# Kernel tuning notes

Measured on AMD Instinct MI355X. Metric: run time of the kernel, lower is better.

## Reference

```python
import jax, jax.numpy as jnp
import numpy as np

EMBED = 768; HEADS = 12; DH = 64; DEPTH = 6; MLP = 3072
PATCH = (4, 16, 16)
N_PATCH = 2048          # (32/4)*(256/16)*(256/16)
N_REAL = N_PATCH + 1    # + cls token
S_PAD = 4096            # padded to multiple of max segment length
SEGS = [128, 256, 512, 1024, 2048]
RATIOS = [1, 2, 4, 8, 16]
NEG = -1e9


def _ln(x, w, b, eps=1e-5):
    m = jnp.mean(x, -1, keepdims=True)
    v = jnp.mean((x - m) ** 2, -1, keepdims=True)
    return (x - m) / jnp.sqrt(v + eps) * w + b


def dilated_attn(x, wq, bq, wk, bk, wv, bv, wo, bo):
    """LongNet dilated attention: per (segment w, ratio r) branch, split the
    sequence into segments of length w, keep every r-th token with a per-head
    offset (h % r), run dense attention inside the sparse segment, then combine
    branches per position/head with softmax-denominator (lse) weights."""
    B, S, E = x.shape
    q = (x @ wq + bq).reshape(B, S, HEADS, DH)
    k = (x @ wk + bk).reshape(B, S, HEADS, DH)
    v = (x @ wv + bv).reshape(B, S, HEADS, DH)
    scale = 1.0 / np.sqrt(DH).astype(np.float32)
    harr = jnp.arange(HEADS)[:, None]
    outs, lses = [], []
    for w, r in zip(SEGS, RATIOS):
        ns, m = S // w, w // r
        idx = (jnp.arange(HEADS)[:, None] % r) + r * jnp.arange(m)[None, :]  # [H, m]

        def seg(t):
            t = t.reshape(B, ns, w, HEADS, DH).transpose(0, 1, 3, 2, 4)  # B,ns,H,w,D
            return jnp.take_along_axis(t, idx[None, None, :, :, None], axis=3)

        qs, ks, vs = seg(q), seg(k), seg(v)  # [B, ns, H, m, D]
        pos = (jnp.arange(ns) * w)[:, None, None] + idx[None]  # [ns, H, m]
        kmask = jnp.where(pos < N_REAL, 0.0, NEG)  # mask padded keys
        sc = jnp.einsum('bnhqd,bnhkd->bnhqk', qs, ks) * scale + kmask[None, :, :, None, :]
        lse = jax.nn.logsumexp(sc, axis=-1)  # [B, ns, H, m]
        o = jnp.einsum('bnhqk,bnhkd->bnhqd', jax.nn.softmax(sc, axis=-1), vs)
        of = jnp.zeros((B, ns, HEADS, w, DH), x.dtype).at[:, :, harr, idx, :].set(o)
        lf = jnp.full((B, ns, HEADS, w), NEG, x.dtype).at[:, :, harr, idx].set(lse)
        outs.append(of.transpose(0, 1, 3, 2, 4).reshape(B, S, HEADS, DH))
        lses.append(lf.transpose(0, 1, 3, 2).reshape(B, S, HEADS))
    O = jnp.stack(outs)   # [Br, B, S, H, D]
    L = jnp.stack(lses)   # [Br, B, S, H]
    wts = jnp.exp(L - jnp.max(L, 0))
    wts = wts / jnp.sum(wts, 0)
    out = jnp.sum(O * wts[..., None], 0).reshape(B, S, E)
    return out @ wo + bo


def setup_inputs() -> dict:
    key = jax.random.key(0)
    ks = jax.random.split(key, 16)
    f = lambda k, shape: (0.02 * jax.random.normal(k, shape)).astype(jnp.float32)
    z = lambda *s: jnp.zeros(s, jnp.float32)
    o = lambda *s: jnp.ones(s, jnp.float32)
    return {
        'x': jax.random.normal(ks[0], (1, 1, 32, 256, 256), dtype=jnp.float32),
        'conv_w': f(ks[1], (EMBED, 1) + PATCH),
        'conv_b': z(EMBED),
        'cls_token': f(ks[2], (1, 1, EMBED)),
        'pos_embed': f(ks[3], (1, N_REAL, EMBED)),
        'ln1_w': o(DEPTH, EMBED), 'ln1_b': z(DEPTH, EMBED),
        'wq': f(ks[4], (DEPTH, EMBED, EMBED)), 'bq': z(DEPTH, EMBED),
        'wk': f(ks[5], (DEPTH, EMBED, EMBED)), 'bk': z(DEPTH, EMBED),
        'wv': f(ks[6], (DEPTH, EMBED, EMBED)), 'bv': z(DEPTH, EMBED),
        'wo': f(ks[7], (DEPTH, EMBED, EMBED)), 'bo': z(DEPTH, EMBED),
        'ln2_w': o(DEPTH, EMBED), 'ln2_b': z(DEPTH, EMBED),
        'w1': f(ks[8], (DEPTH, EMBED, MLP)), 'b1': z(DEPTH, MLP),
        'w2': f(ks[9], (DEPTH, MLP, EMBED)), 'b2': z(DEPTH, EMBED),
        'lnf_w': o(EMBED), 'lnf_b': z(EMBED),
    }


def reference(x, conv_w, conv_b, cls_token, pos_embed, ln1_w, ln1_b,
              wq, bq, wk, bk, wv, bv, wo, bo, ln2_w, ln2_b,
              w1, b1, w2, b2, lnf_w, lnf_b):
    # 3D patch embed: Conv3d stride=kernel=patch, then flatten spatial -> tokens
    p = jax.lax.conv_general_dilated(
        x, conv_w, window_strides=PATCH, padding='VALID',
        dimension_numbers=('NCDHW', 'OIDHW', 'NCDHW'))
    p = p + conv_b[None, :, None, None, None]
    B = p.shape[0]
    tok = p.reshape(B, EMBED, -1).transpose(0, 2, 1)  # [B, N_PATCH, E]
    tok = tok + pos_embed[:, 1:, :]
    cls = cls_token + pos_embed[:, :1, :]
    h = jnp.concatenate([jnp.broadcast_to(cls, (B, 1, EMBED)), tok], axis=1)
    h = jnp.pad(h, ((0, 0), (0, S_PAD - N_REAL), (0, 0)))  # pad to segment multiple

    params = {'ln1_w': ln1_w, 'ln1_b': ln1_b, 'wq': wq, 'bq': bq, 'wk': wk,
              'bk': bk, 'wv': wv, 'bv': bv, 'wo': wo, 'bo': bo,
              'ln2_w': ln2_w, 'ln2_b': ln2_b, 'w1': w1, 'b1': b1,
              'w2': w2, 'b2': b2}

    def layer(h, pr):
        a = dilated_attn(_ln(h, pr['ln1_w'], pr['ln1_b']),
                         pr['wq'], pr['bq'], pr['wk'], pr['bk'],
                         pr['wv'], pr['bv'], pr['wo'], pr['bo'])
        h = h + a
        f = _ln(h, pr['ln2_w'], pr['ln2_b'])
        f = jax.nn.gelu(f @ pr['w1'] + pr['b1'], approximate=False) @ pr['w2'] + pr['b2']
        return h + f, None

    h, _ = jax.lax.scan(layer, h, params)
    return _ln(h[:, 0], lnf_w, lnf_b)  # [B, EMBED]
```

## Files before the change

### kernel.cpp

```cpp
#include <hip/hip_runtime.h>
#include <math.h>

#define EMBED 768
#define HEADS 12
#define DH 64
#define DEPTH 6
#define MLP_DIM 3072
#define N_REAL 2049
#define SP 2112
#define SPAD 2176
#define NEGV (-1e9f)

typedef __attribute__((ext_vector_type(8))) short short8;
typedef __attribute__((ext_vector_type(4))) float f32x4;

__device__ __forceinline__ unsigned short f2bf(float f) {
    union { float f; unsigned u; } x; x.f = f;
    unsigned r = x.u + 0x7FFF + ((x.u >> 16) & 1);
    return (unsigned short)(r >> 16);
}
__device__ __forceinline__ float bf2f(unsigned short s) {
    union { unsigned u; float f; } x; x.u = (unsigned)s << 16;
    return x.f;
}

__device__ __forceinline__ size_t pidx(int mj, int k, int nkt) {
    return (((size_t)(mj >> 4) * nkt + (k >> 5)) << 9) + (size_t)((((k >> 3) & 3) * 16 + (mj & 15)) * 8 + (k & 7));
}

__global__ void im2col_kernel(const float* __restrict__ x, unsigned short* __restrict__ p) {
    const int pi = blockIdx.x;
    const int d = pi >> 8, rr = (pi >> 4) & 15, cc = pi & 15;
    const int t = threadIdx.x;
    #pragma unroll
    for (int u = 0; u < 4; ++u) {
        int i = u * 256 + t;
        int kd = i >> 8, kr = (i >> 4) & 15, kc = i & 15;
        float v = x[(size_t)(d * 4 + kd) * 65536 + (rr * 16 + kr) * 256 + (cc * 16 + kc)];
        p[pidx(pi, i, 32)] = f2bf(v);
    }
}

__device__ __forceinline__ void pack_KN_body(const float* __restrict__ src,
                                             unsigned short* __restrict__ dst,
                                             int N, int K, int bn, int bk) {
    __shared__ float lf[128][33];
    const int t = threadIdx.x;
    {
        const int kk = t >> 3, ch = t & 7;
        const float4* s = (const float4*)(src + (size_t)(bk * 32 + kk) * N + bn * 128 + ch * 16);
        float4 v0 = s[0], v1 = s[1], v2 = s[2], v3 = s[3];
        float tmp[16];
        ((float4*)tmp)[0] = v0; ((float4*)tmp)[1] = v1; ((float4*)tmp)[2] = v2; ((float4*)tmp)[3] = v3;
        #pragma unroll
        for (int u = 0; u < 16; ++u) lf[ch * 16 + u][kk] = tmp[u];
    }
    __syncthreads();
    const int nkt = K >> 5;
    const int cg = t >> 5;
    const int l0 = (t & 31) * 2;
    unsigned short* o = dst + (((size_t)(bn * 8 + cg) * nkt + bk) << 9);
    #pragma unroll
    for (int q = 0; q < 2; ++q) {
        const int l = l0 + q;
        const int col = cg * 16 + (l & 15), kb = (l >> 4) * 8;
        unsigned short ov[8];
        #pragma unroll
        for (int e = 0; e < 8; ++e) ov[e] = f2bf(lf[col][kb + e]);
        *(short8*)(o + l * 8) = *(short8*)ov;
    }
}

__device__ __forceinline__ void pack_piece(int r,
                                           const float* wq, const float* wk,
                                           const float* wv, const float* wo,
                                           const float* w1s, const float* w2s,
                                           unsigned short* qkv_pk, unsigned short* o_pk,
                                           unsigned short* w1_pk, unsigned short* w2_pk) {
    if (r < 576) {
        const int m = r / 144, rr = r % 144;
        const float* src = (m == 0) ? wq : (m == 1) ? wk : (m == 2) ? wv : wo;
        unsigned short* dst = (m < 3) ? qkv_pk + (size_t)m * EMBED * EMBED : o_pk;
        pack_KN_body(src, dst, EMBED, EMBED, rr % 6, rr / 6);
    } else if (r < 1152) {
        const int rr = r - 576;
        pack_KN_body(w1s, w1_pk, MLP_DIM, EMBED, rr % 24, rr / 24);
    } else {
        const int rr = r - 1152;
        pack_KN_body(w2s, w2_pk, EMBED, MLP_DIM, rr % 6, rr / 6);
    }
}

__global__ void pack_all_kernel(const float* __restrict__ wq, const float* __restrict__ wk,
                                const float* __restrict__ wv, const float* __restrict__ wo,
                                const float* __restrict__ w1s, const float* __restrict__ w2s,
                                unsigned short* __restrict__ qkv_pk, unsigned short* __restrict__ o_pk,
                                unsigned short* __restrict__ w1_pk, unsigned short* __restrict__ w2_pk) {
    pack_piece(blockIdx.x, wq, wk, wv, wo, w1s, w2s, qkv_pk, o_pk, w1_pk, w2_pk);
}

__global__ void pack_mega_kernel(const float* __restrict__ wq, const float* __restrict__ wk,
                                 const float* __restrict__ wv, const float* __restrict__ wo,
                                 const float* __restrict__ w1s, const float* __restrict__ w2s,
                                 unsigned short* __restrict__ qkv_pk, unsigned short* __restrict__ o_pk,
                                 unsigned short* __restrict__ w1_pk, unsigned short* __restrict__ w2_pk) {
    const int lid = blockIdx.x / 1728;
    const int r = blockIdx.x % 1728;
    const size_t EE = (size_t)EMBED * EMBED, EM = (size_t)EMBED * MLP_DIM;
    pack_piece(r, wq + lid * EE, wk + lid * EE, wv + lid * EE, wo + lid * EE,
               w1s + lid * EM, w2s + lid * EM,
               qkv_pk + (size_t)lid * 3 * EE, o_pk + lid * EE,
               w1_pk + lid * EM, w2_pk + lid * EM);
}

__global__ void pack_NK_kernel(const float* __restrict__ src, unsigned short* __restrict__ dst,
                               int N, int K) {
    __shared__ float lf[128][33];
    const int bn = blockIdx.x, bk = blockIdx.y;
    const int t = threadIdx.x;
    {
        const int row = t >> 1, hf = t & 1;
        const float4* s = (const float4*)(src + (size_t)(bn * 128 + row) * K + bk * 32 + hf * 16);
        float4 v0 = s[0], v1 = s[1], v2 = s[2], v3 = s[3];
        float tmp[16];
        ((float4*)tmp)[0] = v0; ((float4*)tmp)[1] = v1; ((float4*)tmp)[2] = v2; ((float4*)tmp)[3] = v3;
        #pragma unroll
        for (int u = 0; u < 16; ++u) lf[row][hf * 16 + u] = tmp[u];
    }
    __syncthreads();
    const int nkt = K >> 5;
    const int cg = t >> 5;
    const int l0 = (t & 31) * 2;
    unsigned short* o = dst + (((size_t)(bn * 8 + cg) * nkt + bk) << 9);
    #pragma unroll
    for (int q = 0; q < 2; ++q) {
        const int l = l0 + q;
        const int col = cg * 16 + (l & 15), kb = (l >> 4) * 8;
        unsigned short ov[8];
        #pragma unroll
        for (int e = 0; e < 8; ++e) ov[e] = f2bf(lf[col][kb + e]);
        *(short8*)(o + l * 8) = *(short8*)ov;
    }
}

__global__ void init_misc_kernel(const float* __restrict__ bq, const float* __restrict__ bk,
                                 const float* __restrict__ bv, float* __restrict__ bqkv,
                                 const float* __restrict__ cls, const float* __restrict__ pos,
                                 float* __restrict__ h) {
    int i = blockIdx.x * 256 + threadIdx.x;
    if (i < DEPTH * 2304) {
        int L = i / 2304, j = i - L * 2304;
        float v = (j < 768) ? bq[L * 768 + j] : (j < 1536) ? bk[L * 768 + j - 768] : bv[L * 768 + j - 1536];
        bqkv[i] = v;
    }
    int j = i - DEPTH * 2304;
    if (j >= 0 && j < EMBED) h[j] = cls[j] + pos[j];
}

__global__ void embed_add_kernel(const float* __restrict__ pos, const float* __restrict__ tmp,
                                 float* __restrict__ h) {
    int gid = blockIdx.x * 256 + threadIdx.x;
    if (gid >= 2048 * EMBED) return;
    float v = pos[EMBED + gid];
    #pragma unroll
    for (int c = 0; c < 4; ++c) v += tmp[(size_t)c * SP * EMBED + gid];
    h[EMBED + gid] = v;
}

template<bool PACKED>
__global__ void ln_kernel(const float* __restrict__ in, void* __restrict__ outv,
                          const float* __restrict__ w, const float* __restrict__ b,
                          int M) {
    int row = blockIdx.x;
    if (row >= M) return;
    const float* xr = in + (size_t)row * EMBED;
    int tid = threadIdx.x;
    float v0 = xr[tid], v1 = xr[tid + 256], v2 = xr[tid + 512];
    __shared__ float red[4];
    float s = v0 + v1 + v2;
    #pragma unroll
    for (int o = 32; o > 0; o >>= 1) s += __shfl_down(s, o);
    if ((tid & 63) == 0) red[tid >> 6] = s;
    __syncthreads();
    float mean = (red[0] + red[1] + red[2] + red[3]) * (1.0f / 768.0f);
    __syncthreads();
    float d0 = v0 - mean, d1 = v1 - mean, d2 = v2 - mean;
    float q2 = d0 * d0 + d1 * d1 + d2 * d2;
    #pragma unroll
    for (int o = 32; o > 0; o >>= 1) q2 += __shfl_down(q2, o);
    if ((tid & 63) == 0) red[tid >> 6] = q2;
    __syncthreads();
    float var = (red[0] + red[1] + red[2] + red[3]) * (1.0f / 768.0f);
    float rstd = 1.0f / sqrtf(var + 1e-5f);
    float o0 = d0 * rstd * w[tid]       + b[tid];
    float o1 = d1 * rstd * w[tid + 256] + b[tid + 256];
    float o2 = d2 * rstd * w[tid + 512] + b[tid + 512];
    if (PACKED) {
        unsigned short* o = (unsigned short*)outv;
        o[pidx(row, tid,       24)] = f2bf(o0);
        o[pidx(row, tid + 256, 24)] = f2bf(o1);
        o[pidx(row, tid + 512, 24)] = f2bf(o2);
    } else {
        float* orow = (float*)outv + (size_t)row * EMBED;
        orow[tid] = o0; orow[tid + 256] = o1; orow[tid + 512] = o2;
    }
}

template<bool PACKED>
__global__ void ln_res_kernel(float* __restrict__ h, const float* __restrict__ tmp, int nt,
                              void* __restrict__ outv,
                              const float* __restrict__ w, const float* __restrict__ b,
                              int M) {
    int row = blockIdx.x;
    if (row >= M) return;
    const size_t base = (size_t)row * EMBED;
    int tid = threadIdx.x;
    float v0 = h[base + tid], v1 = h[base + tid + 256], v2 = h[base + tid + 512];
    for (int c = 0; c < nt; ++c) {
        const float* tc = tmp + (size_t)c * SP * EMBED + base;
        v0 += tc[tid]; v1 += tc[tid + 256]; v2 += tc[tid + 512];
    }
    h[base + tid] = v0; h[base + tid + 256] = v1; h[base + tid + 512] = v2;
    __shared__ float red[4];
    float s = v0 + v1 + v2;
    #pragma unroll
    for (int o = 32; o > 0; o >>= 1) s += __shfl_down(s, o);
    if ((tid & 63) == 0) red[tid >> 6] = s;
    __syncthreads();
    float mean = (red[0] + red[1] + red[2] + red[3]) * (1.0f / 768.0f);
    __syncthreads();
    float d0 = v0 - mean, d1 = v1 - mean, d2 = v2 - mean;
    float q2 = d0 * d0 + d1 * d1 + d2 * d2;
    #pragma unroll
    for (int o = 32; o > 0; o >>= 1) q2 += __shfl_down(q2, o);
    if ((tid & 63) == 0) red[tid >> 6] = q2;
    __syncthreads();
    float var = (red[0] + red[1] + red[2] + red[3]) * (1.0f / 768.0f);
    float rstd = 1.0f / sqrtf(var + 1e-5f);
    float o0 = d0 * rstd * w[tid]       + b[tid];
    float o1 = d1 * rstd * w[tid + 256] + b[tid + 256];
    float o2 = d2 * rstd * w[tid + 512] + b[tid + 512];
    if (PACKED) {
        unsigned short* o = (unsigned short*)outv;
        o[pidx(row, tid,       24)] = f2bf(o0);
        o[pidx(row, tid + 256, 24)] = f2bf(o1);
        o[pidx(row, tid + 512, 24)] = f2bf(o2);
    } else {
        float* orow = (float*)outv + (size_t)row * EMBED;
        orow[tid] = o0; orow[tid + 256] = o1; orow[tid + 512] = o2;
    }
}

template<int ACT, int MODE>
__global__ __launch_bounds__(256)
void gemm_bf16(const unsigned short* __restrict__ Apk, const unsigned short* __restrict__ Bpk,
               const float* __restrict__ bias, void* __restrict__ Cv,
               int M, int N, int K, int nx, int ny, int nz) {
    const int nwg = nx * ny * nz;
    const int fid = blockIdx.x;
    const int xcd = fid & 7, slot = fid >> 3;
    const int qq = nwg >> 3, rr2 = nwg & 7;
    const int orig = (xcd < rr2 ? xcd * (qq + 1) : rr2 * (qq + 1) + (xcd - rr2) * qq) + slot;
    const int bx = orig % nx;
    const int tzy = orig / nx;
    const int bz = tzy % nz;
    const int by = tzy / nz;

    const int tid = threadIdx.x;
    const int lane = tid & 63;
    const int w4 = tid >> 6;
    const int wm = w4 >> 1, wn = w4 & 1;
    const int row0 = by * 128 + wm * 64, col0 = bx * 128 + wn * 64;
    const int nktT = K >> 5;
    const int nk = nktT / nz;
    const int t0 = bz * nk;

    f32x4 acc[4][4];
    #pragma unroll
    for (int mi = 0; mi < 4; ++mi)
        #pragma unroll
        for (int ni = 0; ni < 4; ++ni)
            #pragma unroll
            for (int j = 0; j < 4; ++j) acc[mi][ni][j] = 0.0f;

    const unsigned short* Ab[4];
    const unsigned short* Bb[4];
    #pragma unroll
    for (int i = 0; i < 4; ++i) {
        Ab[i] = Apk + (((size_t)(by * 8 + wm * 4 + i) * nktT + t0) << 9) + lane * 8;
        Bb[i] = Bpk + (((size_t)(bx * 8 + wn * 4 + i) * nktT + t0) << 9) + lane * 8;
    }

    auto LOADT = [&](int t, short8* aa, short8* bb) {
        #pragma unroll
        for (int i = 0; i < 4; ++i) {
            aa[i] = *(const short8*)(Ab[i] + (size_t)t * 512);
            bb[i] = *(const short8*)(Bb[i] + (size_t)t * 512);
        }
    };
    auto MF = [&](short8* aa, short8* bb) {
        #pragma unroll
        for (int mi = 0; mi < 4; ++mi)
            #pragma unroll
            for (int ni = 0; ni < 4; ++ni)
                acc[mi][ni] = __builtin_amdgcn_mfma_f32_16x16x32_bf16(aa[mi], bb[ni], acc[mi][ni], 0, 0, 0);
    };

    short8 A0[4], B0[4], A1[4], B1[4];
    LOADT(0, A0, B0);
    for (int t = 0; t < nk; t += 2) {
        LOADT(t + 1, A1, B1);
        MF(A0, B0);
        if (t + 2 < nk) LOADT(t + 2, A0, B0);
        MF(A1, B1);
    }

    float* Cf = (float*)Cv + (MODE == 0 ? (size_t)bz * SP * EMBED : 0);
    unsigned short* Cb = (unsigned short*)Cv;
    const int ln15 = lane & 15, kq = lane >> 4;
    const int nktN = N >> 5;
    const bool addb = (bz == 0);
    #pragma unroll
    for (int mi = 0; mi < 4; ++mi) {
        #pragma unroll
        for (int ni = 0; ni < 4; ++ni) {
            const int col = col0 + ni * 16 + ln15;
            const float bb = addb ? bias[col] : 0.0f;
            #pragma unroll
            for (int j = 0; j < 4; ++j) {
                const int row = row0 + mi * 16 + kq * 4 + j;
                if (row < M) {
                    float v = acc[mi][ni][j] + bb;
                    if (ACT == 1) v = 0.5f * v * (1.0f + erff(v * 0.70710678118654752f));
                    if (MODE == 0)      Cf[(size_t)row * N + col] = v;
                    else if (MODE == 2) Cb[(size_t)row * N + col] = f2bf(v);
                    else                Cb[pidx(row, col, nktN)] = f2bf(v);
                }
            }
        }
    }
}

__global__ __launch_bounds__(256, 1)
void attn_kernel(const unsigned short* __restrict__ qkv,
                 unsigned short* __restrict__ Obr, float* __restrict__ Lbr) {
    const int bx = blockIdx.x, hh = blockIdx.y;
    int b, n;
    if      (bx < 17) { b = 0; n = bx; }
    else if (bx < 26) { b = 1; n = bx - 17; }
    else if (bx < 31) { b = 2; n = bx - 26; }
    else if (bx < 34) { b = 3; n = bx - 31; }
    else              { b = 4; n = bx - 34; }
    const int r = 1 << b;
    const int segw = 128 << b;
    const int base = n * segw + (hh & (r - 1));

    __shared__ __attribute__((aligned(16))) unsigned short VT[64 * 128];
    __shared__ __attribute__((aligned(16))) unsigned short Pl[128 * 128];

    const int tid = threadIdx.x;

    {
        const int key = tid >> 1, dh2 = (tid & 1) * 32;
        const int pos = base + r * key;
        const bool val = pos < N_REAL;
        const unsigned short* vsrc = qkv + (size_t)(val ? pos : 0) * 2304 + 1536 + hh * 64 + dh2;
        #pragma unroll
        for (int u = 0; u < 4; ++u) {
            short8 vv = ((const short8*)vsrc)[u];
            #pragma unroll
            for (int e = 0; e < 8; ++e) {
                const int d = dh2 + u * 8 + e;
                VT[(d * 256 + ((key * 2) ^ ((d & 7) << 4))) >> 1] =
                    val ? (unsigned short)vv[e] : (unsigned short)0;
            }
        }
    }
    __syncthreads();

    const int lane = tid & 63, wv = tid >> 6;
    const int ln15 = lane & 15, kq = lane >> 4;

    f32x4 sc[2][8];
    #pragma unroll
    for (int mi = 0; mi < 2; ++mi)
        #pragma unroll
        for (int ni = 0; ni < 8; ++ni)
            #pragma unroll
            for (int j = 0; j < 4; ++j) sc[mi][ni][j] = 0.0f;

    #pragma unroll
    for (int kt = 0; kt < 2; ++kt) {
        short8 qfr[2], kfr[8];
        #pragma unroll
        for (int mi = 0; mi < 2; ++mi) {
            const int pos = base + r * (wv * 32 + mi * 16 + ln15);
            qfr[mi] = *(const short8*)(qkv + (size_t)(pos < N_REAL ? pos : 0) * 2304
                                       + hh * 64 + kt * 32 + kq * 8);
        }
        #pragma unroll
        for (int ni = 0; ni < 8; ++ni) {
            const int pos = base + r * (ni * 16 + ln15);
            kfr[ni] = *(const short8*)(qkv + (size_t)(pos < N_REAL ? pos : 0) * 2304
                                       + 768 + hh * 64 + kt * 32 + kq * 8);
        }
        #pragma unroll
        for (int mi = 0; mi < 2; ++mi)
            #pragma unroll
            for (int ni = 0; ni < 8; ++ni)
                sc[mi][ni] = __builtin_amdgcn_mfma_f32_16x16x32_bf16(qfr[mi], kfr[ni], sc[mi][ni], 0, 0, 0);
    }

    #pragma unroll
    for (int ni = 0; ni < 8; ++ni) {
        const bool kval = (base + r * (ni * 16 + ln15)) < N_REAL;
        #pragma unroll
        for (int mi = 0; mi < 2; ++mi)
            #pragma unroll
            for (int j = 0; j < 4; ++j)
                sc[mi][ni][j] = kval ? sc[mi][ni][j] * 0.125f : NEGV;
    }

    float rsum[2][4];
    #pragma unroll
    for (int mi = 0; mi < 2; ++mi) {
        #pragma unroll
        for (int j = 0; j < 4; ++j) {
            float mx = sc[mi][0][j];
            #pragma unroll
            for (int ni = 1; ni < 8; ++ni) mx = fmaxf(mx, sc[mi][ni][j]);
            mx = fmaxf(mx, __shfl_xor(mx, 1));
            mx = fmaxf(mx, __shfl_xor(mx, 2));
            mx = fmaxf(mx, __shfl_xor(mx, 4));
            mx = fmaxf(mx, __shfl_xor(mx, 8));
            float sm = 0.f;
            #pragma unroll
            for (int ni = 0; ni < 8; ++ni) {
                float e = __expf(sc[mi][ni][j] - mx);
                sc[mi][ni][j] = e;
                sm += e;
            }
            sm += __shfl_xor(sm, 1);
            sm += __shfl_xor(sm, 2);
            sm += __shfl_xor(sm, 4);
            sm += __shfl_xor(sm, 8);
            rsum[mi][j] = sm;
            const int prow = wv * 32 + mi * 16 + kq * 4 + j;
            const int qpos = base + r * prow;
            if (ln15 == 0 && qpos < N_REAL)
                Lbr[((size_t)b * SP + qpos) * HEADS + hh] = mx + logf(sm);
        }
    }

    #pragma unroll
    for (int mi = 0; mi < 2; ++mi)
        #pragma unroll
        for (int j = 0; j < 4; ++j) {
            const int prow = wv * 32 + mi * 16 + kq * 4 + j;
            #pragma unroll
            for (int ni = 0; ni < 8; ++ni) {
                const int col = ni * 16 + ln15;
                Pl[(prow * 256 + ((col * 2) ^ ((prow & 7) << 4))) >> 1] = f2bf(sc[mi][ni][j]);
            }
        }
    __syncthreads();

    f32x4 ov[2][4];
    #pragma unroll
    for (int mi = 0; mi < 2; ++mi)
        #pragma unroll
        for (int ni = 0; ni < 4; ++ni)
            #pragma unroll
            for (int j = 0; j < 4; ++j) ov[mi][ni][j] = 0.0f;

    #pragma unroll
    for (int kt = 0; kt < 4; ++kt) {
        short8 pa[2], vb[4];
        #pragma unroll
        for (int mi = 0; mi < 2; ++mi) {
            const int row = wv * 32 + mi * 16 + ln15;
            pa[mi] = *(const short8*)((const char*)Pl + row * 256
                                      + ((kt * 64 + kq * 16) ^ ((row & 7) << 4)));
        }
        #pragma unroll
        for (int ni = 0; ni < 4; ++ni) {
            const int d = ni * 16 + ln15;
            vb[ni] = *(const short8*)((const char*)VT + d * 256
                                      + ((kt * 64 + kq * 16) ^ ((d & 7) << 4)));
        }
        #pragma unroll
        for (int mi = 0; mi < 2; ++mi)
            #pragma unroll
            for (int ni = 0; ni < 4; ++ni)
                ov[mi][ni] = __builtin_amdgcn_mfma_f32_16x16x32_bf16(pa[mi], vb[ni], ov[mi][ni], 0, 0, 0);
    }

    #pragma unroll
    for (int mi = 0; mi < 2; ++mi)
        #pragma unroll
        for (int j = 0; j < 4; ++j) {
            const int prow = wv * 32 + mi * 16 + kq * 4 + j;
            const int qpos = base + r * prow;
            if (qpos < N_REAL) {
                const float inv = 1.0f / rsum[mi][j];
                #pragma unroll
                for (int ni = 0; ni < 4; ++ni)
                    Obr[((size_t)b * N_REAL + qpos) * EMBED + hh * 64 + ni * 16 + ln15] =
                        f2bf(ov[mi][ni][j] * inv);
            }
        }
}

__global__ void combine_kernel(const unsigned short* __restrict__ Obr, const float* __restrict__ Lbr,
                               unsigned short* __restrict__ out) {
    int gid = blockIdx.x * 256 + threadIdx.x;
    if (gid >= N_REAL * EMBED) return;
    int p = gid / EMBED, e = gid - p * EMBED;
    int h = e >> 6;
    float l[5];
    float mx = NEGV;
    #pragma unroll
    for (int b = 0; b < 5; ++b) {
        const int rm = (1 << b) - 1;
        l[b] = ((p & rm) == (h & rm)) ? Lbr[((size_t)b * SP + p) * HEADS + h] : NEGV;
        mx = fmaxf(mx, l[b]);
    }
    float wsum = 0.f, acc = 0.f;
    #pragma unroll
    for (int b = 0; b < 5; ++b) {
        if (l[b] > NEGV * 0.5f) {
            float wt = expf(l[b] - mx);
            wsum += wt;
            acc += wt * bf2f(Obr[((size_t)b * N_REAL + p) * EMBED + e]);
        }
    }
    out[pidx(p, e, 24)] = f2bf(acc / wsum);
}

extern "C" void kernel_launch(void* const* d_in, const int* in_sizes, int n_in,
                              void* d_out, int out_size, void* d_ws, size_t ws_size,
                              hipStream_t stream) {
    const float* x      = (const float*)d_in[0];
    const float* conv_w = (const float*)d_in[1];
    const float* conv_b = (const float*)d_in[2];
    const float* cls    = (const float*)d_in[3];
    const float* pos    = (const float*)d_in[4];
    const float* ln1w   = (const float*)d_in[5];
    const float* ln1b   = (const float*)d_in[6];
    const float* wq     = (const float*)d_in[7];
    const float* bq     = (const float*)d_in[8];
    const float* wk     = (const float*)d_in[9];
    const float* bk     = (const float*)d_in[10];
    const float* wv     = (const float*)d_in[11];
    const float* bv     = (const float*)d_in[12];
    const float* wo     = (const float*)d_in[13];
    const float* bo     = (const float*)d_in[14];
    const float* ln2w   = (const float*)d_in[15];
    const float* ln2b   = (const float*)d_in[16];
    const float* w1     = (const float*)d_in[17];
    const float* b1     = (const float*)d_in[18];
    const float* w2     = (const float*)d_in[19];
    const float* b2     = (const float*)d_in[20];
    const float* lnfw   = (const float*)d_in[21];
    const float* lnfb   = (const float*)d_in[22];

    const size_t EE = (size_t)EMBED * EMBED;
    const size_t EM = (size_t)EMBED * MLP_DIM;

    const size_t base_floats =
        (size_t)SP * EMBED
        + 4 * (size_t)SP * EMBED
        + 5 * (size_t)SP * HEADS
        + (size_t)DEPTH * 2304
        + (size_t)SPAD * 2304 / 2
        + (size_t)SPAD * EMBED / 2
        + (size_t)SPAD * EMBED / 2
        + (size_t)SPAD * MLP_DIM / 2
        + (size_t)2112 * 1024 / 2
        + (size_t)EMBED * 1024 / 2
        + ((size_t)5 * N_REAL * EMBED / 2 + 64);
    const size_t per_layer_floats = (3 * EE + EE + EM + EM) / 2;
    const bool up = ws_size >= (base_floats + 6 * per_layer_floats) * 4 + (1 << 20);
    const int NL = up ? DEPTH : 1;

    float* ws = (float*)d_ws;
    float* h     = ws;  ws += (size_t)SP * EMBED;
    float* tmp   = ws;  ws += (size_t)4 * SP * EMBED;
    float* Lbr   = ws;  ws += (size_t)5 * SP * HEADS;
    float* bqkv  = ws;  ws += (size_t)DEPTH * 2304;
    unsigned short* qkv_bf   = (unsigned short*)ws;  ws += (size_t)SPAD * 2304 / 2;
    unsigned short* xln_pk   = (unsigned short*)ws;  ws += (size_t)SPAD * EMBED / 2;
    unsigned short* attn_pk  = (unsigned short*)ws;  ws += (size_t)SPAD * EMBED / 2;
    unsigned short* mid_pk   = (unsigned short*)ws;  ws += (size_t)SPAD * MLP_DIM / 2;
    unsigned short* patch_pk = (unsigned short*)ws;  ws += (size_t)2112 * 1024 / 2;
    unsigned short* convw_pk = (unsigned short*)ws;  ws += (size_t)EMBED * 1024 / 2;
    unsigned short* Obr      = (unsigned short*)ws;  ws += (size_t)5 * N_REAL * EMBED / 2 + 64;
    unsigned short* wqkv_pk  = (unsigned short*)ws;  ws += (size_t)NL * 3 * EE / 2;
    unsigned short* wo_pk    = (unsigned short*)ws;  ws += (size_t)NL * EE / 2;
    unsigned short* w1_pk    = (unsigned short*)ws;  ws += (size_t)NL * EM / 2;
    unsigned short* w2_pk    = (unsigned short*)ws;  ws += (size_t)NL * EM / 2;

    im2col_kernel<<<2048, 256, 0, stream>>>(x, patch_pk);
    pack_NK_kernel<<<dim3(6, 32), 256, 0, stream>>>(conv_w, convw_pk, EMBED, 1024);
    init_misc_kernel<<<(DEPTH * 2304 + EMBED + 255) / 256, 256, 0, stream>>>(
        bq, bk, bv, bqkv, cls, pos, h);
    if (up)
        pack_mega_kernel<<<DEPTH * 1728, 256, 0, stream>>>(wq, wk, wv, wo, w1, w2,
                                                           wqkv_pk, wo_pk, w1_pk, w2_pk);
    gemm_bf16<0, 0><<<384, 256, 0, stream>>>(patch_pk, convw_pk, conv_b,
                                             tmp, 2048, EMBED, 1024, 6, 16, 4);
    embed_add_kernel<<<(2048 * EMBED + 255) / 256, 256, 0, stream>>>(pos, tmp, h);

    for (int L = 0; L < DEPTH; ++L) {
        const int off = up ? L : 0;
        unsigned short* qkvW = wqkv_pk + (size_t)off * 3 * EE;
        unsigned short* woW  = wo_pk   + (size_t)off * EE;
        unsigned short* w1W  = w1_pk   + (size_t)off * EM;
        unsigned short* w2W  = w2_pk   + (size_t)off * EM;
        if (!up)
            pack_all_kernel<<<1728, 256, 0, stream>>>(wq + L * EE, wk + L * EE, wv + L * EE,
                                                      wo + L * EE, w1 + L * EM, w2 + L * EM,
                                                      qkvW, woW, w1W, w2W);

        if (L == 0)
            ln_kernel<true><<<N_REAL, 256, 0, stream>>>(h, xln_pk, ln1w + (size_t)L * EMBED,
                                                        ln1b + (size_t)L * EMBED, N_REAL);
        else
            ln_res_kernel<true><<<N_REAL, 256, 0, stream>>>(h, tmp, 4, xln_pk,
                                                            ln1w + (size_t)L * EMBED,
                                                            ln1b + (size_t)L * EMBED, N_REAL);
        gemm_bf16<0, 2><<<306, 256, 0, stream>>>(xln_pk, qkvW, bqkv + (size_t)L * 2304,
                                                 qkv_bf, N_REAL, 2304, EMBED, 18, 17, 1);
        attn_kernel<<<dim3(36, 12), 256, 0, stream>>>(qkv_bf, Obr, Lbr);
        combine_kernel<<<((N_REAL * EMBED) + 255) / 256, 256, 0, stream>>>(Obr, Lbr, attn_pk);
        gemm_bf16<0, 0><<<408, 256, 0, stream>>>(attn_pk, woW, bo + (size_t)L * EMBED,
                                                 tmp, N_REAL, EMBED, EMBED, 6, 17, 4);
        ln_res_kernel<true><<<N_REAL, 256, 0, stream>>>(h, tmp, 4, xln_pk,
                                                        ln2w + (size_t)L * EMBED,
                                                        ln2b + (size_t)L * EMBED, N_REAL);
        gemm_bf16<1, 3><<<408, 256, 0, stream>>>(xln_pk, w1W, b1 + (size_t)L * MLP_DIM,
                                                 mid_pk, N_REAL, MLP_DIM, EMBED, 24, 17, 1);
        gemm_bf16<0, 0><<<408, 256, 0, stream>>>(mid_pk, w2W, b2 + (size_t)L * EMBED,
                                                 tmp, N_REAL, EMBED, MLP_DIM, 6, 17, 4);
    }

    ln_res_kernel<false><<<1, 256, 0, stream>>>(h, tmp, 4, (float*)d_out, lnfw, lnfb, 1);
}
```

Baseline: 929.1 us.

## Merge all prep kernels into one launch, swizzle pack LDS, use polynomial GELU

Combines the im2col, conv-weight packing, bias/cls init and per-layer weight packing into a single prep_mega_kernel launch, dispatched by block index, so there are fewer launches and the small kernels no longer serialize. The LDS writes in pack_KN_body are rotated by column group to reduce bank conflicts during the transpose. The exact erff in the GELU epilogue is replaced with an Abramowitz-Stegun polynomial with __expf, which is cheaper but less accurate (about 1e-7 absolute error).

Result: faster. 907.8 us, median of 2 (-2.3%).

```diff
diff --git a/kernel.cpp b/kernel.cpp
--- a/kernel.cpp
+++ b/kernel.cpp
@@ -24,12 +24,22 @@
     return x.f;
 }
 
+__device__ __forceinline__ float fast_gelu(float v) {
+    const float ax = fabsf(v) * 0.70710678118654752f;
+    const float tt = 1.0f / (1.0f + 0.3275911f * ax);
+    const float poly = tt * (0.254829592f + tt * (-0.284496736f + tt * (1.421413741f
+                       + tt * (-1.453152027f + tt * 1.061405429f))));
+    float er = 1.0f - poly * __expf(-ax * ax);
+    er = (v < 0.0f) ? -er : er;
+    return 0.5f * v * (1.0f + er);
+}
+
 __device__ __forceinline__ size_t pidx(int mj, int k, int nkt) {
     return (((size_t)(mj >> 4) * nkt + (k >> 5)) << 9) + (size_t)((((k >> 3) & 3) * 16 + (mj & 15)) * 8 + (k & 7));
 }
 
-__global__ void im2col_kernel(const float* __restrict__ x, unsigned short* __restrict__ p) {
-    const int pi = blockIdx.x;
+__device__ __forceinline__ void im2col_body(const float* __restrict__ x,
+                                            unsigned short* __restrict__ p, int pi) {
     const int d = pi >> 8, rr = (pi >> 4) & 15, cc = pi & 15;
     const int t = threadIdx.x;
     #pragma unroll
@@ -39,6 +49,10 @@
         float v = x[(size_t)(d * 4 + kd) * 65536 + (rr * 16 + kr) * 256 + (cc * 16 + kc)];
         p[pidx(pi, i, 32)] = f2bf(v);
     }
+}
+
+__global__ void im2col_kernel(const float* __restrict__ x, unsigned short* __restrict__ p) {
+    im2col_body(x, p, blockIdx.x);
 }
 
 __device__ __forceinline__ void pack_KN_body(const float* __restrict__ src,
@@ -52,13 +66,15 @@
         float4 v0 = s[0], v1 = s[1], v2 = s[2], v3 = s[3];
         float tmp[16];
         ((float4*)tmp)[0] = v0; ((float4*)tmp)[1] = v1; ((float4*)tmp)[2] = v2; ((float4*)tmp)[3] = v3;
-        #pragma unroll
-        for (int u = 0; u < 16; ++u) lf[ch * 16 + u][kk] = tmp[u];
+        const int cidx = (kk + 4 * ch) & 31;
+        #pragma unroll
+        for (int u = 0; u < 16; ++u) lf[ch * 16 + u][cidx] = tmp[u];
     }
     __syncthreads();
     const int nkt = K >> 5;
     const int cg = t >> 5;
     const int l0 = (t & 31) * 2;
+    const int rot = 4 * cg;
     unsigned short* o = dst + (((size_t)(bn * 8 + cg) * nkt + bk) << 9);
     #pragma unroll
     for (int q = 0; q < 2; ++q) {
@@ -66,7 +82,7 @@
         const int col = cg * 16 + (l & 15), kb = (l >> 4) * 8;
         unsigned short ov[8];
         #pragma unroll
-        for (int e = 0; e < 8; ++e) ov[e] = f2bf(lf[col][kb + e]);
+        for (int e = 0; e < 8; ++e) ov[e] = f2bf(lf[col][(kb + e + rot) & 31]);
         *(short8*)(o + l * 8) = *(short8*)ov;
     }
 }
@@ -99,24 +115,10 @@
     pack_piece(blockIdx.x, wq, wk, wv, wo, w1s, w2s, qkv_pk, o_pk, w1_pk, w2_pk);
 }
 
-__global__ void pack_mega_kernel(const float* __restrict__ wq, const float* __restrict__ wk,
-                                 const float* __restrict__ wv, const float* __restrict__ wo,
-                                 const float* __restrict__ w1s, const float* __restrict__ w2s,
-                                 unsigned short* __restrict__ qkv_pk, unsigned short* __restrict__ o_pk,
-                                 unsigned short* __restrict__ w1_pk, unsigned short* __restrict__ w2_pk) {
-    const int lid = blockIdx.x / 1728;
-    const int r = blockIdx.x % 1728;
-    const size_t EE = (size_t)EMBED * EMBED, EM = (size_t)EMBED * MLP_DIM;
-    pack_piece(r, wq + lid * EE, wk + lid * EE, wv + lid * EE, wo + lid * EE,
-               w1s + lid * EM, w2s + lid * EM,
-               qkv_pk + (size_t)lid * 3 * EE, o_pk + lid * EE,
-               w1_pk + lid * EM, w2_pk + lid * EM);
-}
-
-__global__ void pack_NK_kernel(const float* __restrict__ src, unsigned short* __restrict__ dst,
-                               int N, int K) {
+__device__ __forceinline__ void pack_NK_body(const float* __restrict__ src,
+                                             unsigned short* __restrict__ dst,
+                                             int N, int K, int bn, int bk) {
     __shared__ float lf[128][33];
-    const int bn = blockIdx.x, bk = blockIdx.y;
     const int t = threadIdx.x;
     {
         const int row = t >> 1, hf = t & 1;
@@ -143,18 +145,61 @@
     }
 }
 
+__global__ void pack_NK_kernel(const float* __restrict__ src, unsigned short* __restrict__ dst,
+                               int N, int K) {
+    pack_NK_body(src, dst, N, K, blockIdx.x, blockIdx.y);
+}
+
+__device__ __forceinline__ void init_misc_body(int i,
+                                 const float* __restrict__ bq, const float* __restrict__ bk,
+                                 const float* __restrict__ bv, float* __restrict__ bqkv,
+                                 const float* __restrict__ cls, const float* __restrict__ pos,
+                                 float* __restrict__ h) {
+    if (i < DEPTH * 2304) {
+        int L = i / 2304, j = i - L * 2304;
+        float v = (j < 768) ? bq[L * 768 + j] : (j < 1536) ? bk[L * 768 + j - 768] : bv[L * 768 + j - 1536];
+        bqkv[i] = v;
+    }
+    int j = i - DEPTH * 2304;
+    if (j >= 0 && j < EMBED) h[j] = cls[j] + pos[j];
+}
+
 __global__ void init_misc_kernel(const float* __restrict__ bq, const float* __restrict__ bk,
                                  const float* __restrict__ bv, float* __restrict__ bqkv,
                                  const float* __restrict__ cls, const float* __restrict__ pos,
                                  float* __restrict__ h) {
-    int i = blockIdx.x * 256 + threadIdx.x;
-    if (i < DEPTH * 2304) {
-        int L = i / 2304, j = i - L * 2304;
-        float v = (j < 768) ? bq[L * 768 + j] : (j < 1536) ? bk[L * 768 + j - 768] : bv[L * 768 + j - 1536];
-        bqkv[i] = v;
-    }
-    int j = i - DEPTH * 2304;
-    if (j >= 0 && j < EMBED) h[j] = cls[j] + pos[j];
+    init_misc_body(blockIdx.x * 256 + threadIdx.x, bq, bk, bv, bqkv, cls, pos, h);
+}
+
+__global__ void prep_mega_kernel(const float* __restrict__ x, const float* __restrict__ conv_w,
+                                 const float* __restrict__ wq, const float* __restrict__ wk,
+                                 const float* __restrict__ wv, const float* __restrict__ wo,
+                                 const float* __restrict__ w1s, const float* __restrict__ w2s,
+                                 const float* __restrict__ bq, const float* __restrict__ bk,
+                                 const float* __restrict__ bv, const float* __restrict__ cls,
+                                 const float* __restrict__ pos,
+                                 unsigned short* __restrict__ patch_pk,
+                                 unsigned short* __restrict__ convw_pk,
+                                 float* __restrict__ bqkv, float* __restrict__ h,
+                                 unsigned short* __restrict__ qkv_pk, unsigned short* __restrict__ o_pk,
+                                 unsigned short* __restrict__ w1_pk, unsigned short* __restrict__ w2_pk) {
+    const int fid = blockIdx.x;
+    const size_t EE = (size_t)EMBED * EMBED, EM = (size_t)EMBED * MLP_DIM;
+    if (fid < 6 * 1728) {
+        const int lid = fid / 1728, r = fid % 1728;
+        pack_piece(r, wq + lid * EE, wk + lid * EE, wv + lid * EE, wo + lid * EE,
+                   w1s + lid * EM, w2s + lid * EM,
+                   qkv_pk + (size_t)lid * 3 * EE, o_pk + lid * EE,
+                   w1_pk + lid * EM, w2_pk + lid * EM);
+    } else if (fid < 6 * 1728 + 192) {
+        const int r = fid - 6 * 1728;
+        pack_NK_body(conv_w, convw_pk, EMBED, 1024, r % 6, r / 6);
+    } else if (fid < 6 * 1728 + 192 + 2048) {
+        im2col_body(x, patch_pk, fid - (6 * 1728 + 192));
+    } else {
+        const int r = fid - (6 * 1728 + 192 + 2048);
+        init_misc_body(r * 256 + threadIdx.x, bq, bk, bv, bqkv, cls, pos, h);
+    }
 }
 
 __global__ void embed_add_kernel(const float* __restrict__ pos, const float* __restrict__ tmp,
@@ -331,7 +376,7 @@
                 const int row = row0 + mi * 16 + kq * 4 + j;
                 if (row < M) {
                     float v = acc[mi][ni][j] + bb;
-                    if (ACT == 1) v = 0.5f * v * (1.0f + erff(v * 0.70710678118654752f));
+                    if (ACT == 1) v = fast_gelu(v);
                     if (MODE == 0)      Cf[(size_t)row * N + col] = v;
                     else if (MODE == 2) Cb[(size_t)row * N + col] = f2bf(v);
                     else                Cb[pidx(row, col, nktN)] = f2bf(v);
@@ -568,17 +613,10 @@
     const size_t EM = (size_t)EMBED * MLP_DIM;
 
     const size_t base_floats =
-        (size_t)SP * EMBED
-        + 4 * (size_t)SP * EMBED
-        + 5 * (size_t)SP * HEADS
-        + (size_t)DEPTH * 2304
-        + (size_t)SPAD * 2304 / 2
-        + (size_t)SPAD * EMBED / 2
-        + (size_t)SPAD * EMBED / 2
-        + (size_t)SPAD * MLP_DIM / 2
-        + (size_t)2112 * 1024 / 2
-        + (size_t)EMBED * 1024 / 2
-        + ((size_t)5 * N_REAL * EMBED / 2 + 64);
+        (size_t)SP * EMBED + 4 * (size_t)SP * EMBED + 5 * (size_t)SP * HEADS
+        + (size_t)DEPTH * 2304 + (size_t)SPAD * 2304 / 2 + (size_t)SPAD * EMBED / 2
+        + (size_t)SPAD * EMBED / 2 + (size_t)SPAD * MLP_DIM / 2 + (size_t)2112 * 1024 / 2
+        + (size_t)EMBED * 1024 / 2 + ((size_t)5 * N_REAL * EMBED / 2 + 64);
     const size_t per_layer_floats = (3 * EE + EE + EM + EM) / 2;
     const bool up = ws_size >= (base_floats + 6 * per_layer_floats) * 4 + (1 << 20);
     const int NL = up ? DEPTH : 1;
@@ -600,13 +638,16 @@
     unsigned short* w1_pk    = (unsigned short*)ws;  ws += (size_t)NL * EM / 2;
     unsigned short* w2_pk    = (unsigned short*)ws;  ws += (size_t)NL * EM / 2;
 
-    im2col_kernel<<<2048, 256, 0, stream>>>(x, patch_pk);
-    pack_NK_kernel<<<dim3(6, 32), 256, 0, stream>>>(conv_w, convw_pk, EMBED, 1024);
-    init_misc_kernel<<<(DEPTH * 2304 + EMBED + 255) / 256, 256, 0, stream>>>(
-        bq, bk, bv, bqkv, cls, pos, h);
-    if (up)
-        pack_mega_kernel<<<DEPTH * 1728, 256, 0, stream>>>(wq, wk, wv, wo, w1, w2,
-                                                           wqkv_pk, wo_pk, w1_pk, w2_pk);
+    if (up) {
+        prep_mega_kernel<<<6 * 1728 + 192 + 2048 + 57, 256, 0, stream>>>(
+            x, conv_w, wq, wk, wv, wo, w1, w2, bq, bk, bv, cls, pos,
+            patch_pk, convw_pk, bqkv, h, wqkv_pk, wo_pk, w1_pk, w2_pk);
+    } else {
+        im2col_kernel<<<2048, 256, 0, stream>>>(x, patch_pk);
+        pack_NK_kernel<<<dim3(6, 32), 256, 0, stream>>>(conv_w, convw_pk, EMBED, 1024);
+        init_misc_kernel<<<(DEPTH * 2304 + EMBED + 255) / 256, 256, 0, stream>>>(
+            bq, bk, bv, bqkv, cls, pos, h);
+    }
     gemm_bf16<0, 0><<<384, 256, 0, stream>>>(patch_pk, convw_pk, conv_b,
                                              tmp, 2048, EMBED, 1024, 6, 16, 4);
     embed_add_kernel<<<(2048 * EMBED + 255) / 256, 256, 0, stream>>>(pos, tmp, h);
```
